# Kernel tuning notes

Hardware: AMD Instinct MI355X
Metric: run time of the kernel (lower is better)

Reference implementation:

```python
import jax, jax.numpy as jnp
import numpy as np

N = 4096  # num_neurons
THRESHOLD = 0.0  # torch forward default


def setup_inputs() -> dict:
    key = jax.random.key(0)
    k1, k2 = jax.random.split(key)
    W = jax.random.normal(k1, (N, N), dtype=jnp.float32)
    # Hopfield weights have zero self-connections (fill_diagonal_(0))
    W = W * (1.0 - jnp.eye(N, dtype=jnp.float32))
    x = jax.random.normal(k2, (N,), dtype=jnp.float32)
    return {"input_pattern": x, "weights": W, "max_iterations": 4}


def reference(input_pattern, weights, max_iterations):
    n = weights.shape[0]

    # One asynchronous neuron update: uses the CURRENT (partially updated) state.
    def neuron_step(state, i):
        activation = jnp.dot(weights[i], state)  # row-i dot current state
        state = state.at[i].set(jnp.sign(activation - THRESHOLD))
        return state, None

    # One full sweep over all neurons, in order 0..n-1 (asynchronous updates).
    def sweep(state, _):
        state, _ = jax.lax.scan(neuron_step, state, jnp.arange(n))
        return state, None

    # Fixed number of sweeps. A converged state is a fixed point of `sweep`,
    # so this matches the torch early-break loop's final output exactly.
    state, _ = jax.lax.scan(sweep, input_pattern, None, length=max_iterations)
    return state
```

## Files before the change

### kernel.cpp

```cpp
#include <hip/hip_runtime.h>

#define NN 4096
#define BB 128
#define GG 32
#define MAXT 8
#define MAXE (MAXT * GG)
#define MASK63 0x7FFFFFFFFFFFFFFFull
#define MASK62 0x3FFFFFFFFFFFFFFFull
#define TOPBIT 0x8000000000000000ull

__global__ __launch_bounds__(256)
void hop_init(const float* __restrict__ x, const float* __restrict__ W,
              unsigned long long* __restrict__ slots, float* __restrict__ partial_buf)
{
    const int tid = threadIdx.x, bid = blockIdx.x;
    const int lane = tid & 63, w = tid >> 6;
    const int lam = lane & 31, half = lane >> 5;

    if (bid == 0) {
        for (int i = tid; i < MAXE * 8; i += 256) slots[i] = 0ull;
    }

    const int tm = bid >> 3, tc = bid & 7;
    const int rbase = tm * BB, cbase = tc * 512;

    float4 xv[4];
#pragma unroll
    for (int u = 0; u < 4; ++u)
        xv[u] = *(const float4*)(x + cbase + 4 * lam + 128 * u);

#pragma unroll 2
    for (int it = 0; it < 16; ++it) {
        const int r = w * 32 + it * 2 + half;
        const float* wrow = W + (size_t)(rbase + r) * NN + cbase;
        float p = 0.f;
#pragma unroll
        for (int u = 0; u < 4; ++u) {
            float4 wv = *(const float4*)(wrow + 4 * lam + 128 * u);
            p = fmaf(wv.x, xv[u].x, p); p = fmaf(wv.y, xv[u].y, p);
            p = fmaf(wv.z, xv[u].z, p); p = fmaf(wv.w, xv[u].w, p);
        }
#pragma unroll
        for (int s = 16; s; s >>= 1) p += __shfl_xor(p, s);
        if (lam == 0) partial_buf[(size_t)bid * BB + r] = p;
    }
}

__global__ __launch_bounds__(256)
void hop_main(const float* __restrict__ x, const float* __restrict__ W,
              const int* __restrict__ maxit, float* __restrict__ out,
              unsigned long long* __restrict__ slots,
              const float* __restrict__ partial_buf)
{
    __shared__ float wdT[BB][BB + 1];
    __shared__ float a_lds[BB];
    __shared__ float prev_lds[NN];
    __shared__ float delta_lds[BB];
    __shared__ int   status_lds;
    __shared__ int   nzw[2][4];

    const int tid = threadIdx.x;
    const int m = blockIdx.x;
    const int lane = tid & 63, w = tid >> 6;
    const int lam = lane & 31, half = lane >> 5;
    const int bm = m * BB;

    int T = *maxit; if (T > MAXT) T = MAXT; if (T < 0) T = 0;
    const long long tstart = clock64();

    for (int l = tid; l < BB * BB; l += 256) {
        const int i = l >> 7, j = l & 127;
        wdT[j][i] = W[(size_t)(bm + i) * NN + bm + j];
    }
    for (int i = tid; i < NN; i += 256) prev_lds[i] = x[i];
    if (tid < BB) {
        float s = 0.f;
#pragma unroll
        for (int c = 0; c < 8; ++c) s += partial_buf[(size_t)(m * 8 + c) * BB + tid];
        a_lds[tid] = s;
    }
    float sold0 = 0.f, sold1 = 0.f;
    if (w == 0) { sold0 = x[bm + lane]; sold1 = x[bm + 64 + lane]; }
    __syncthreads();

    for (int e = 0; e < T * GG; ++e) {
        const int k = e & (GG - 1);
        if (k != m) {
            float4 wpre[16];
#pragma unroll
            for (int it = 0; it < 16; ++it) {
                const int r = w * 32 + it * 2 + half;
                wpre[it] = *(const float4*)(W + (size_t)(bm + r) * NN + k * BB + 4 * lam);
            }
            const unsigned long long* sl = slots + (size_t)e * 8;
            unsigned long long q0, q1, q2;
            int iters = 0;
            for (;;) {
                q0 = __hip_atomic_load(&sl[0], __ATOMIC_RELAXED, __HIP_MEMORY_SCOPE_AGENT);
                q1 = __hip_atomic_load(&sl[1], __ATOMIC_RELAXED, __HIP_MEMORY_SCOPE_AGENT);
                q2 = __hip_atomic_load(&sl[2], __ATOMIC_RELAXED, __HIP_MEMORY_SCOPE_AGENT);
                if ((q0 & q1 & q2) >> 63) break;
                __builtin_amdgcn_s_sleep(1);
                if (((++iters) & 255) == 0 && (clock64() - tstart) > 2000000000LL) break;
            }
            const unsigned long long m0 = (q0 & MASK63) | (q1 << 63);
            const unsigned long long m1 = ((q1 >> 1) & MASK62) | (q2 << 62);

            const int jc = 4 * lam;
            const float4 pv = *(const float4*)&prev_lds[k * BB + jc];
            float4 d4;
            {
                const float s0 = ((jc + 0 < 64 ? (m0 >> (jc + 0)) : (m1 >> (jc - 64))) & 1) ? 1.f : -1.f;
                const float s1 = ((jc + 1 < 64 ? (m0 >> (jc + 1)) : (m1 >> (jc - 63))) & 1) ? 1.f : -1.f;
                const float s2 = ((jc + 2 < 64 ? (m0 >> (jc + 2)) : (m1 >> (jc - 62))) & 1) ? 1.f : -1.f;
                const float s3 = ((jc + 3 < 64 ? (m0 >> (jc + 3)) : (m1 >> (jc - 61))) & 1) ? 1.f : -1.f;
                d4.x = s0 - pv.x; d4.y = s1 - pv.y; d4.z = s2 - pv.z; d4.w = s3 - pv.w;
            }
            const bool nz = (d4.x != 0.f) || (d4.y != 0.f) || (d4.z != 0.f) || (d4.w != 0.f);
            const unsigned long long bnz = __ballot(nz);
            if (lane == 0) nzw[e & 1][w] = (bnz != 0ull);
            __syncthreads();
            if (tid < BB) {
                const int b = tid < 64 ? (int)((m0 >> tid) & 1) : (int)((m1 >> (tid - 64)) & 1);
                prev_lds[k * BB + tid] = b ? 1.f : -1.f;
            }
            const int any = nzw[e & 1][0] | nzw[e & 1][1] | nzw[e & 1][2] | nzw[e & 1][3];
            if (any) {
#pragma unroll
                for (int it = 0; it < 16; ++it) {
                    const int r = w * 32 + it * 2 + half;
                    const float4 wv = wpre[it];
                    float p = fmaf(wv.x, d4.x, fmaf(wv.y, d4.y, fmaf(wv.z, d4.z, wv.w * d4.w)));
#pragma unroll
                    for (int s = 16; s; s >>= 1) p += __shfl_xor(p, s);
                    if (lam == 0) a_lds[r] += p;
                }
            }
        } else {
            __syncthreads();
            if (w == 0) {
                float c0 = a_lds[lane], c1 = a_lds[lane + 64];
                const float dp0 = 1.f - sold0, dm0 = -1.f - sold0;
                const float dp1 = 1.f - sold1, dm1 = -1.f - sold1;
                const float cand0 = c0 > 0.f ? dp0 : dm0;
                const float cand1 = c1 > 0.f ? dp1 : dm1;
                const unsigned long long bz = __ballot((cand0 != 0.f) || (cand1 != 0.f));
                float vdf0 = 0.f, vdf1 = 0.f;
                const int zero_all = (bz == 0ULL);
                if (!zero_all) {
                    float vsn0 = sold0, vsn1 = sold1;
                    float pw0[6], pw1[6];
#pragma unroll
                    for (int u = 0; u < 6; ++u) { pw0[u] = wdT[u][lane]; pw1[u] = wdT[u][lane + 64]; }
#pragma unroll
                    for (int j = 0; j < 64; ++j) {
                        const float dq = c0 > 0.f ? dp0 : dm0;
                        const float sq = c0 > 0.f ? 1.f : -1.f;
                        const float bc = __int_as_float(
                            __builtin_amdgcn_readlane(__float_as_int(dq), j));
                        const bool me = (lane == j);
                        vdf0 = me ? dq : vdf0;
                        vsn0 = me ? sq : vsn0;
                        const float w0 = pw0[j % 6], w1 = pw1[j % 6];
                        pw0[j % 6] = wdT[j + 6][lane];
                        pw1[j % 6] = wdT[j + 6][lane + 64];
                        c0 = fmaf(w0, bc, c0);
                        c1 = fmaf(w1, bc, c1);
                    }
                    const float cnd1 = c1 > 0.f ? dp1 : dm1;
                    const unsigned long long bz1 = __ballot(cnd1 != 0.f);
                    if (bz1 != 0ULL) {
#pragma unroll
                        for (int j = 64; j < 128; ++j) {
                            const float dq = c1 > 0.f ? dp1 : dm1;
                            const float sq = c1 > 0.f ? 1.f : -1.f;
                            const float bc = __int_as_float(
                                __builtin_amdgcn_readlane(__float_as_int(dq), j & 63));
                            const bool me = (lane == (j & 63));
                            vdf1 = me ? dq : vdf1;
                            vsn1 = me ? sq : vsn1;
                            const float w1 = pw1[j % 6];
                            if (j + 6 < BB) pw1[j % 6] = wdT[j + 6][lane + 64];
                            c1 = fmaf(w1, bc, c1);
                        }
                    }
                    sold0 = vsn0;
                    sold1 = vsn1;
                }
                {
                    const unsigned long long m0 = __ballot(sold0 > 0.f);
                    const unsigned long long m1 = __ballot(sold1 > 0.f);
                    unsigned long long* sl = slots + (size_t)e * 8;
                    if (lane == 0) {
                        __hip_atomic_store(&sl[0], TOPBIT | (m0 & MASK63),
                                           __ATOMIC_RELAXED, __HIP_MEMORY_SCOPE_AGENT);
                        __hip_atomic_store(&sl[1], TOPBIT | (m0 >> 63) | ((m1 & MASK62) << 1),
                                           __ATOMIC_RELAXED, __HIP_MEMORY_SCOPE_AGENT);
                        __hip_atomic_store(&sl[2], TOPBIT | (m1 >> 62),
                                           __ATOMIC_RELAXED, __HIP_MEMORY_SCOPE_AGENT);
                    }
                }
                if (lane == 0) status_lds = zero_all;
                if (!zero_all) {
                    delta_lds[lane] = vdf0;
                    delta_lds[lane + 64] = vdf1;
                }
            }
            __syncthreads();
            if (!status_lds) {
                float dv[4];
#pragma unroll
                for (int u = 0; u < 4; ++u) dv[u] = delta_lds[lam + 32 * u];
#pragma unroll 2
                for (int it = 0; it < 16; ++it) {
                    const int r = w * 32 + it * 2 + half;
                    float p = 0.f;
#pragma unroll
                    for (int u = 0; u < 4; ++u) p = fmaf(wdT[lam + 32 * u][r], dv[u], p);
#pragma unroll
                    for (int s = 16; s; s >>= 1) p += __shfl_xor(p, s);
                    if (lam == 0) a_lds[r] += p;
                }
            }
        }
    }

    if (w == 0) {
        out[bm + lane] = sold0;
        out[bm + 64 + lane] = sold1;
    }
}

extern "C" void kernel_launch(void* const* d_in, const int* in_sizes, int n_in,
                              void* d_out, int out_size, void* d_ws, size_t ws_size,
                              hipStream_t stream) {
    const float* x = (const float*)d_in[0];
    const float* W = (const float*)d_in[1];
    const int* maxit = (const int*)d_in[2];
    float* out = (float*)d_out;

    char* ws = (char*)d_ws;
    unsigned long long* slots = (unsigned long long*)ws;
    float* partial_buf = (float*)(ws + (size_t)MAXE * 8 * 8);
    if (ws_size < (size_t)(MAXE * 64 + 256 * BB * 4)) return;

    hipLaunchKernelGGL(hop_init, dim3(256), dim3(256), 0, stream,
                       x, W, slots, partial_buf);

    void* args[6];
    args[0] = (void*)&x; args[1] = (void*)&W; args[2] = (void*)&maxit;
    args[3] = (void*)&out; args[4] = (void*)&slots; args[5] = (void*)&partial_buf;
    (void)hipLaunchCooperativeKernel(hop_main, dim3(GG), dim3(256), args, 0u, stream);
}
```

Measured before the change: 1.103 ms.

## Poll slots from one wave with distance-scaled backoff and double-buffer prev state

Only wave 0 polls the global slot flags, and its sleep interval grows with the ring distance between producer and consumer block; the mask is then passed to the other waves through LDS after a barrier. The skip decision now compares the new mask with the previous sweep's mask kept in LDS, instead of a ballot over deltas and a second barrier. The previous-state array is double-buffered per sweep to avoid a read/write hazard. This aims to cut global polling traffic and barrier overhead on the serial chain, at the cost of more LDS and possible extra latency from longer sleeps.

Result: faster. 1.060 ms (-3.9%).

```diff
diff --git a/kernel.cpp b/kernel.cpp
--- a/kernel.cpp
+++ b/kernel.cpp
@@ -53,11 +53,12 @@
               const float* __restrict__ partial_buf)
 {
     __shared__ float wdT[BB][BB + 1];
+    __shared__ float pbuf[2][NN];
     __shared__ float a_lds[BB];
-    __shared__ float prev_lds[NN];
     __shared__ float delta_lds[BB];
+    __shared__ unsigned long long mbox[2][2];
+    __shared__ unsigned long long pm[2][GG][2];
     __shared__ int   status_lds;
-    __shared__ int   nzw[2][4];
 
     const int tid = threadIdx.x;
     const int m = blockIdx.x;
@@ -72,7 +73,7 @@
         const int i = l >> 7, j = l & 127;
         wdT[j][i] = W[(size_t)(bm + i) * NN + bm + j];
     }
-    for (int i = tid; i < NN; i += 256) prev_lds[i] = x[i];
+    for (int i = tid; i < NN; i += 256) pbuf[0][i] = x[i];
     if (tid < BB) {
         float s = 0.f;
 #pragma unroll
@@ -85,6 +86,7 @@
 
     for (int e = 0; e < T * GG; ++e) {
         const int k = e & (GG - 1);
+        const int s = e >> 5;
         if (k != m) {
             float4 wpre[16];
 #pragma unroll
@@ -92,22 +94,39 @@
                 const int r = w * 32 + it * 2 + half;
                 wpre[it] = *(const float4*)(W + (size_t)(bm + r) * NN + k * BB + 4 * lam);
             }
-            const unsigned long long* sl = slots + (size_t)e * 8;
-            unsigned long long q0, q1, q2;
-            int iters = 0;
-            for (;;) {
-                q0 = __hip_atomic_load(&sl[0], __ATOMIC_RELAXED, __HIP_MEMORY_SCOPE_AGENT);
-                q1 = __hip_atomic_load(&sl[1], __ATOMIC_RELAXED, __HIP_MEMORY_SCOPE_AGENT);
-                q2 = __hip_atomic_load(&sl[2], __ATOMIC_RELAXED, __HIP_MEMORY_SCOPE_AGENT);
-                if ((q0 & q1 & q2) >> 63) break;
-                __builtin_amdgcn_s_sleep(1);
-                if (((++iters) & 255) == 0 && (clock64() - tstart) > 2000000000LL) break;
-            }
-            const unsigned long long m0 = (q0 & MASK63) | (q1 << 63);
-            const unsigned long long m1 = ((q1 >> 1) & MASK62) | (q2 << 62);
+            if (w == 0) {
+                const unsigned long long* sl = slots + (size_t)e * 8;
+                const int dist = (m - k + GG) & (GG - 1);
+                unsigned long long q0, q1, q2;
+                long long iters = 0;
+                for (;;) {
+                    q0 = __hip_atomic_load(&sl[0], __ATOMIC_RELAXED, __HIP_MEMORY_SCOPE_AGENT);
+                    q1 = __hip_atomic_load(&sl[1], __ATOMIC_RELAXED, __HIP_MEMORY_SCOPE_AGENT);
+                    q2 = __hip_atomic_load(&sl[2], __ATOMIC_RELAXED, __HIP_MEMORY_SCOPE_AGENT);
+                    if ((q0 & q1 & q2) >> 63) break;
+                    if (dist == 1)      __builtin_amdgcn_s_sleep(1);
+                    else if (dist <= 4) __builtin_amdgcn_s_sleep(4);
+                    else                __builtin_amdgcn_s_sleep(32);
+                    if (((++iters) & 63) == 0 && (clock64() - tstart) > 500000000LL) break;
+                }
+                const unsigned long long mm0 = (q0 & MASK63) | (q1 << 63);
+                const unsigned long long mm1 = ((q1 >> 1) & MASK62) | (q2 << 62);
+                if (lane == 0) {
+                    mbox[e & 1][0] = mm0;
+                    mbox[e & 1][1] = mm1;
+                    pm[s & 1][k][0] = mm0;
+                    pm[s & 1][k][1] = mm1;
+                }
+            }
+            __syncthreads();
+            const unsigned long long m0 = mbox[e & 1][0];
+            const unsigned long long m1 = mbox[e & 1][1];
+            const bool any = (s == 0) ||
+                             (m0 != pm[(s - 1) & 1][k][0]) ||
+                             (m1 != pm[(s - 1) & 1][k][1]);
 
             const int jc = 4 * lam;
-            const float4 pv = *(const float4*)&prev_lds[k * BB + jc];
+            const float4 pv = *(const float4*)&pbuf[s & 1][k * BB + jc];
             float4 d4;
             {
                 const float s0 = ((jc + 0 < 64 ? (m0 >> (jc + 0)) : (m1 >> (jc - 64))) & 1) ? 1.f : -1.f;
@@ -116,15 +135,10 @@
                 const float s3 = ((jc + 3 < 64 ? (m0 >> (jc + 3)) : (m1 >> (jc - 61))) & 1) ? 1.f : -1.f;
                 d4.x = s0 - pv.x; d4.y = s1 - pv.y; d4.z = s2 - pv.z; d4.w = s3 - pv.w;
             }
-            const bool nz = (d4.x != 0.f) || (d4.y != 0.f) || (d4.z != 0.f) || (d4.w != 0.f);
-            const unsigned long long bnz = __ballot(nz);
-            if (lane == 0) nzw[e & 1][w] = (bnz != 0ull);
-            __syncthreads();
             if (tid < BB) {
                 const int b = tid < 64 ? (int)((m0 >> tid) & 1) : (int)((m1 >> (tid - 64)) & 1);
-                prev_lds[k * BB + tid] = b ? 1.f : -1.f;
-            }
-            const int any = nzw[e & 1][0] | nzw[e & 1][1] | nzw[e & 1][2] | nzw[e & 1][3];
+                pbuf[(s + 1) & 1][k * BB + tid] = b ? 1.f : -1.f;
+            }
             if (any) {
 #pragma unroll
                 for (int it = 0; it < 16; ++it) {
@@ -132,7 +146,7 @@
                     const float4 wv = wpre[it];
                     float p = fmaf(wv.x, d4.x, fmaf(wv.y, d4.y, fmaf(wv.z, d4.z, wv.w * d4.w)));
 #pragma unroll
-                    for (int s = 16; s; s >>= 1) p += __shfl_xor(p, s);
+                    for (int sh = 16; sh; sh >>= 1) p += __shfl_xor(p, sh);
                     if (lam == 0) a_lds[r] += p;
                 }
             }
@@ -188,15 +202,15 @@
                     sold1 = vsn1;
                 }
                 {
-                    const unsigned long long m0 = __ballot(sold0 > 0.f);
-                    const unsigned long long m1 = __ballot(sold1 > 0.f);
+                    const unsigned long long pm0 = __ballot(sold0 > 0.f);
+                    const unsigned long long pm1 = __ballot(sold1 > 0.f);
                     unsigned long long* sl = slots + (size_t)e * 8;
                     if (lane == 0) {
-                        __hip_atomic_store(&sl[0], TOPBIT | (m0 & MASK63),
+                        __hip_atomic_store(&sl[0], TOPBIT | (pm0 & MASK63),
                                            __ATOMIC_RELAXED, __HIP_MEMORY_SCOPE_AGENT);
-                        __hip_atomic_store(&sl[1], TOPBIT | (m0 >> 63) | ((m1 & MASK62) << 1),
+                        __hip_atomic_store(&sl[1], TOPBIT | (pm0 >> 63) | ((pm1 & MASK62) << 1),
                                            __ATOMIC_RELAXED, __HIP_MEMORY_SCOPE_AGENT);
-                        __hip_atomic_store(&sl[2], TOPBIT | (m1 >> 62),
+                        __hip_atomic_store(&sl[2], TOPBIT | (pm1 >> 62),
                                            __ATOMIC_RELAXED, __HIP_MEMORY_SCOPE_AGENT);
                     }
                 }
@@ -218,7 +232,7 @@
 #pragma unroll
                     for (int u = 0; u < 4; ++u) p = fmaf(wdT[lam + 32 * u][r], dv[u], p);
 #pragma unroll
-                    for (int s = 16; s; s >>= 1) p += __shfl_xor(p, s);
+                    for (int sh = 16; sh; sh >>= 1) p += __shfl_xor(p, sh);
                     if (lam == 0) a_lds[r] += p;
                 }
             }
```

## Use 8 large workgroups owning 4 sub-blocks each with pipelined delta application

Applied to the files above, without the earlier changes.

Switches from 32 workgroups of 256 threads, each owning one 128-row block, to 8 workgroups of 1024 threads, each owning 512 rows split into four 128-row sub-blocks. One wavefront polls the flag slots while the other 15 wavefronts apply the previous step's delta to the block's rows, so waiting and computation overlap. The next diagonal block is double-buffered into LDS during the serial update. Deltas are now formed from bitmasks of earlier states, and polling backs off according to how far away the producer is. The aim is fewer cross-workgroup handoffs and hidden polling latency, in exchange for reading W from global memory on every apply and having fewer CUs active.

After: 1.447 ms. +31.2%, slower.

```diff
diff --git a/kernel.cpp b/kernel.cpp
--- a/kernel.cpp
+++ b/kernel.cpp
@@ -1,10 +1,14 @@
 #include <hip/hip_runtime.h>
 
 #define NN 4096
-#define BB 128
-#define GG 32
+#define SB 128
+#define NSB 32
+#define NWG 8
+#define SPW 4
+#define ROWS 512
 #define MAXT 8
-#define MAXE (MAXT * GG)
+#define MAXE (MAXT * NSB)
+#define NTH 1024
 #define MASK63 0x7FFFFFFFFFFFFFFFull
 #define MASK62 0x3FFFFFFFFFFFFFFFull
 #define TOPBIT 0x8000000000000000ull
@@ -22,7 +26,7 @@
     }
 
     const int tm = bid >> 3, tc = bid & 7;
-    const int rbase = tm * BB, cbase = tc * 512;
+    const int rbase = tm * SB, cbase = tc * 512;
 
     float4 xv[4];
 #pragma unroll
@@ -42,104 +46,125 @@
         }
 #pragma unroll
         for (int s = 16; s; s >>= 1) p += __shfl_xor(p, s);
-        if (lam == 0) partial_buf[(size_t)bid * BB + r] = p;
-    }
-}
-
-__global__ __launch_bounds__(256)
+        if (lam == 0) partial_buf[(size_t)bid * SB + r] = p;
+    }
+}
+
+__device__ __forceinline__ void apply_rows(
+    const float* __restrict__ W, int rowbase, float* a_lds,
+    const float* dl_p, int cb, int r0, int r1, int wv, int lam, int half)
+{
+    const float4 d4 = *(const float4*)(dl_p + 4 * lam);
+    const int npairs = (r1 - r0) >> 1;
+    for (int i = wv - 1; i < npairs; i += 15) {
+        const int r = r0 + 2 * i + half;
+        const float* wr = W + (size_t)(rowbase + r) * NN + cb + 4 * lam;
+        const float4 wvv = *(const float4*)wr;
+        float p = fmaf(wvv.x, d4.x, fmaf(wvv.y, d4.y, fmaf(wvv.z, d4.z, wvv.w * d4.w)));
+#pragma unroll
+        for (int sh = 16; sh; sh >>= 1) p += __shfl_xor(p, sh);
+        if (lam == 0) a_lds[r] += p;
+    }
+}
+
+__global__ __launch_bounds__(NTH)
 void hop_main(const float* __restrict__ x, const float* __restrict__ W,
               const int* __restrict__ maxit, float* __restrict__ out,
               unsigned long long* __restrict__ slots,
               const float* __restrict__ partial_buf)
 {
-    __shared__ float wdT[BB][BB + 1];
-    __shared__ float a_lds[BB];
-    __shared__ float prev_lds[NN];
-    __shared__ float delta_lds[BB];
-    __shared__ int   status_lds;
-    __shared__ int   nzw[2][4];
+    __shared__ float wdT[2][SB][SB + 1];
+    __shared__ float x_lds[NN];
+    __shared__ float a_lds[ROWS];
+    __shared__ float sold_lds[ROWS];
+    __shared__ float dl[2][SB];
+    __shared__ unsigned long long pm[2][NSB][2];
+    __shared__ int pend_any[2];
+    __shared__ int pend_cb[2];
 
     const int tid = threadIdx.x;
     const int m = blockIdx.x;
-    const int lane = tid & 63, w = tid >> 6;
+    const int lane = tid & 63, wv = tid >> 6;
     const int lam = lane & 31, half = lane >> 5;
-    const int bm = m * BB;
+    const int rowbase = m * ROWS;
 
     int T = *maxit; if (T > MAXT) T = MAXT; if (T < 0) T = 0;
     const long long tstart = clock64();
 
-    for (int l = tid; l < BB * BB; l += 256) {
+    for (int i = tid; i < NN; i += NTH) x_lds[i] = x[i];
+    for (int l = tid; l < SB * SB; l += NTH) {
         const int i = l >> 7, j = l & 127;
-        wdT[j][i] = W[(size_t)(bm + i) * NN + bm + j];
-    }
-    for (int i = tid; i < NN; i += 256) prev_lds[i] = x[i];
-    if (tid < BB) {
+        wdT[0][j][i] = W[(size_t)(rowbase + i) * NN + rowbase + j];
+    }
+    if (tid < ROWS) {
         float s = 0.f;
 #pragma unroll
-        for (int c = 0; c < 8; ++c) s += partial_buf[(size_t)(m * 8 + c) * BB + tid];
+        for (int c = 0; c < 8; ++c)
+            s += partial_buf[(size_t)((m * SPW + (tid >> 7)) * 8 + c) * SB + (tid & 127)];
         a_lds[tid] = s;
-    }
-    float sold0 = 0.f, sold1 = 0.f;
-    if (w == 0) { sold0 = x[bm + lane]; sold1 = x[bm + 64 + lane]; }
+        sold_lds[tid] = x[rowbase + tid];
+    }
+    if (tid < 2) { pend_any[tid] = 0; pend_cb[tid] = 0; }
+    int cur = 0;
     __syncthreads();
 
-    for (int e = 0; e < T * GG; ++e) {
-        const int k = e & (GG - 1);
-        if (k != m) {
-            float4 wpre[16];
-#pragma unroll
-            for (int it = 0; it < 16; ++it) {
-                const int r = w * 32 + it * 2 + half;
-                wpre[it] = *(const float4*)(W + (size_t)(bm + r) * NN + k * BB + 4 * lam);
+    for (int t = 0; t < T * NSB; ++t) {
+        const int b = t & (NSB - 1);
+        const int s = t >> 5;
+        const int pp = t & 1, qq = pp ^ 1;
+        if ((b >> 2) != m) {
+            if (wv == 0) {
+                const unsigned long long* sl = slots + (size_t)t * 8;
+                const int d = (b < SPW * m) ? (SPW * m - b) : (NSB - b + SPW * m);
+                unsigned long long q0, q1, q2;
+                long long iters = 0;
+                for (;;) {
+                    q0 = __hip_atomic_load(&sl[0], __ATOMIC_RELAXED, __HIP_MEMORY_SCOPE_AGENT);
+                    q1 = __hip_atomic_load(&sl[1], __ATOMIC_RELAXED, __HIP_MEMORY_SCOPE_AGENT);
+                    q2 = __hip_atomic_load(&sl[2], __ATOMIC_RELAXED, __HIP_MEMORY_SCOPE_AGENT);
+                    if ((q0 & q1 & q2) >> 63) break;
+                    if (d == 1)      __builtin_amdgcn_s_sleep(1);
+                    else if (d <= 4) __builtin_amdgcn_s_sleep(4);
+                    else             __builtin_amdgcn_s_sleep(32);
+                    if (((++iters) & 63) == 0 && (clock64() - tstart) > 500000000LL) break;
+                }
+                const unsigned long long mm0 = (q0 & MASK63) | (q1 << 63);
+                const unsigned long long mm1 = ((q1 >> 1) & MASK62) | (q2 << 62);
+                const unsigned long long p0 = pm[(s - 1) & 1][b][0];
+                const unsigned long long p1 = pm[(s - 1) & 1][b][1];
+                const int any = (s == 0) || (mm0 != p0) || (mm1 != p1);
+                {
+                    const int j0 = lane;
+                    const float cur0 = ((mm0 >> j0) & 1) ? 1.f : -1.f;
+                    const float prev0 = (s == 0) ? x_lds[b * SB + j0]
+                                                 : (((p0 >> j0) & 1) ? 1.f : -1.f);
+                    dl[pp][j0] = cur0 - prev0;
+                    const float cur1 = ((mm1 >> j0) & 1) ? 1.f : -1.f;
+                    const float prev1 = (s == 0) ? x_lds[b * SB + 64 + j0]
+                                                 : (((p1 >> j0) & 1) ? 1.f : -1.f);
+                    dl[pp][64 + j0] = cur1 - prev1;
+                }
+                if (lane == 0) {
+                    pm[s & 1][b][0] = mm0;
+                    pm[s & 1][b][1] = mm1;
+                    pend_any[pp] = any;
+                    pend_cb[pp] = b * SB;
+                }
+            } else {
+                if (pend_any[qq])
+                    apply_rows(W, rowbase, a_lds, dl[qq], pend_cb[qq], 0, ROWS, wv, lam, half);
             }
-            const unsigned long long* sl = slots + (size_t)e * 8;
-            unsigned long long q0, q1, q2;
-            int iters = 0;
-            for (;;) {
-                q0 = __hip_atomic_load(&sl[0], __ATOMIC_RELAXED, __HIP_MEMORY_SCOPE_AGENT);
-                q1 = __hip_atomic_load(&sl[1], __ATOMIC_RELAXED, __HIP_MEMORY_SCOPE_AGENT);
-                q2 = __hip_atomic_load(&sl[2], __ATOMIC_RELAXED, __HIP_MEMORY_SCOPE_AGENT);
-                if ((q0 & q1 & q2) >> 63) break;
-                __builtin_amdgcn_s_sleep(1);
-                if (((++iters) & 255) == 0 && (clock64() - tstart) > 2000000000LL) break;
-            }
-            const unsigned long long m0 = (q0 & MASK63) | (q1 << 63);
-            const unsigned long long m1 = ((q1 >> 1) & MASK62) | (q2 << 62);
-
-            const int jc = 4 * lam;
-            const float4 pv = *(const float4*)&prev_lds[k * BB + jc];
-            float4 d4;
-            {
-                const float s0 = ((jc + 0 < 64 ? (m0 >> (jc + 0)) : (m1 >> (jc - 64))) & 1) ? 1.f : -1.f;
-                const float s1 = ((jc + 1 < 64 ? (m0 >> (jc + 1)) : (m1 >> (jc - 63))) & 1) ? 1.f : -1.f;
-                const float s2 = ((jc + 2 < 64 ? (m0 >> (jc + 2)) : (m1 >> (jc - 62))) & 1) ? 1.f : -1.f;
-                const float s3 = ((jc + 3 < 64 ? (m0 >> (jc + 3)) : (m1 >> (jc - 61))) & 1) ? 1.f : -1.f;
-                d4.x = s0 - pv.x; d4.y = s1 - pv.y; d4.z = s2 - pv.z; d4.w = s3 - pv.w;
-            }
-            const bool nz = (d4.x != 0.f) || (d4.y != 0.f) || (d4.z != 0.f) || (d4.w != 0.f);
-            const unsigned long long bnz = __ballot(nz);
-            if (lane == 0) nzw[e & 1][w] = (bnz != 0ull);
             __syncthreads();
-            if (tid < BB) {
-                const int b = tid < 64 ? (int)((m0 >> tid) & 1) : (int)((m1 >> (tid - 64)) & 1);
-                prev_lds[k * BB + tid] = b ? 1.f : -1.f;
-            }
-            const int any = nzw[e & 1][0] | nzw[e & 1][1] | nzw[e & 1][2] | nzw[e & 1][3];
-            if (any) {
-#pragma unroll
-                for (int it = 0; it < 16; ++it) {
-                    const int r = w * 32 + it * 2 + half;
-                    const float4 wv = wpre[it];
-                    float p = fmaf(wv.x, d4.x, fmaf(wv.y, d4.y, fmaf(wv.z, d4.z, wv.w * d4.w)));
-#pragma unroll
-                    for (int s = 16; s; s >>= 1) p += __shfl_xor(p, s);
-                    if (lam == 0) a_lds[r] += p;
-                }
-            }
         } else {
+            const int lb = b & (SPW - 1);
+            if (wv > 0 && pend_any[qq])
+                apply_rows(W, rowbase, a_lds, dl[qq], pend_cb[qq],
+                           lb * SB, lb * SB + SB, wv, lam, half);
             __syncthreads();
-            if (w == 0) {
-                float c0 = a_lds[lane], c1 = a_lds[lane + 64];
+            if (wv == 0) {
+                float (*wd)[SB + 1] = wdT[cur];
+                float c0 = a_lds[lb * SB + lane], c1 = a_lds[lb * SB + 64 + lane];
+                float sold0 = sold_lds[lb * SB + lane], sold1 = sold_lds[lb * SB + 64 + lane];
                 const float dp0 = 1.f - sold0, dm0 = -1.f - sold0;
                 const float dp1 = 1.f - sold1, dm1 = -1.f - sold1;
                 const float cand0 = c0 > 0.f ? dp0 : dm0;
@@ -151,7 +176,7 @@
                     float vsn0 = sold0, vsn1 = sold1;
                     float pw0[6], pw1[6];
 #pragma unroll
-                    for (int u = 0; u < 6; ++u) { pw0[u] = wdT[u][lane]; pw1[u] = wdT[u][lane + 64]; }
+                    for (int u = 0; u < 6; ++u) { pw0[u] = wd[u][lane]; pw1[u] = wd[u][lane + 64]; }
 #pragma unroll
                     for (int j = 0; j < 64; ++j) {
                         const float dq = c0 > 0.f ? dp0 : dm0;
@@ -162,8 +187,8 @@
                         vdf0 = me ? dq : vdf0;
                         vsn0 = me ? sq : vsn0;
                         const float w0 = pw0[j % 6], w1 = pw1[j % 6];
-                        pw0[j % 6] = wdT[j + 6][lane];
-                        pw1[j % 6] = wdT[j + 6][lane + 64];
+                        pw0[j % 6] = wd[j + 6][lane];
+                        pw1[j % 6] = wd[j + 6][lane + 64];
                         c0 = fmaf(w0, bc, c0);
                         c1 = fmaf(w1, bc, c1);
                     }
@@ -180,55 +205,50 @@
                             vdf1 = me ? dq : vdf1;
                             vsn1 = me ? sq : vsn1;
                             const float w1 = pw1[j % 6];
-                            if (j + 6 < BB) pw1[j % 6] = wdT[j + 6][lane + 64];
+                            if (j + 6 < SB) pw1[j % 6] = wd[j + 6][lane + 64];
                             c1 = fmaf(w1, bc, c1);
                         }
                     }
-                    sold0 = vsn0;
-                    sold1 = vsn1;
+                    sold0 = vsn0; sold1 = vsn1;
+                    sold_lds[lb * SB + lane] = sold0;
+                    sold_lds[lb * SB + 64 + lane] = sold1;
                 }
                 {
-                    const unsigned long long m0 = __ballot(sold0 > 0.f);
-                    const unsigned long long m1 = __ballot(sold1 > 0.f);
-                    unsigned long long* sl = slots + (size_t)e * 8;
+                    const unsigned long long b0 = __ballot(sold0 > 0.f);
+                    const unsigned long long b1 = __ballot(sold1 > 0.f);
+                    unsigned long long* sl = slots + (size_t)t * 8;
                     if (lane == 0) {
-                        __hip_atomic_store(&sl[0], TOPBIT | (m0 & MASK63),
+                        __hip_atomic_store(&sl[0], TOPBIT | (b0 & MASK63),
                                            __ATOMIC_RELAXED, __HIP_MEMORY_SCOPE_AGENT);
-                        __hip_atomic_store(&sl[1], TOPBIT | (m0 >> 63) | ((m1 & MASK62) << 1),
+                        __hip_atomic_store(&sl[1], TOPBIT | (b0 >> 63) | ((b1 & MASK62) << 1),
                                            __ATOMIC_RELAXED, __HIP_MEMORY_SCOPE_AGENT);
-                        __hip_atomic_store(&sl[2], TOPBIT | (m1 >> 62),
+                        __hip_atomic_store(&sl[2], TOPBIT | (b1 >> 62),
                                            __ATOMIC_RELAXED, __HIP_MEMORY_SCOPE_AGENT);
                     }
                 }
-                if (lane == 0) status_lds = zero_all;
-                if (!zero_all) {
-                    delta_lds[lane] = vdf0;
-                    delta_lds[lane + 64] = vdf1;
+                dl[pp][lane] = vdf0;
+                dl[pp][lane + 64] = vdf1;
+                if (lane == 0) { pend_any[pp] = !zero_all; pend_cb[pp] = b * SB; }
+            } else {
+                if (pend_any[qq]) {
+                    apply_rows(W, rowbase, a_lds, dl[qq], pend_cb[qq],
+                               0, lb * SB, wv, lam, half);
+                    apply_rows(W, rowbase, a_lds, dl[qq], pend_cb[qq],
+                               lb * SB + SB, ROWS, wv, lam, half);
+                }
+                const int nlb = (lb + 1) & (SPW - 1);
+                const int nb = rowbase + nlb * SB;
+                for (int l = tid - 64; l < SB * SB; l += (NTH - 64)) {
+                    const int i = l >> 7, j = l & 127;
+                    wdT[cur ^ 1][j][i] = W[(size_t)(nb + i) * NN + nb + j];
                 }
             }
             __syncthreads();
-            if (!status_lds) {
-                float dv[4];
-#pragma unroll
-                for (int u = 0; u < 4; ++u) dv[u] = delta_lds[lam + 32 * u];
-#pragma unroll 2
-                for (int it = 0; it < 16; ++it) {
-                    const int r = w * 32 + it * 2 + half;
-                    float p = 0.f;
-#pragma unroll
-                    for (int u = 0; u < 4; ++u) p = fmaf(wdT[lam + 32 * u][r], dv[u], p);
-#pragma unroll
-                    for (int s = 16; s; s >>= 1) p += __shfl_xor(p, s);
-                    if (lam == 0) a_lds[r] += p;
-                }
-            }
+            cur ^= 1;
         }
     }
 
-    if (w == 0) {
-        out[bm + lane] = sold0;
-        out[bm + 64 + lane] = sold1;
-    }
+    if (tid < ROWS) out[rowbase + tid] = sold_lds[tid];
 }
 
 extern "C" void kernel_launch(void* const* d_in, const int* in_sizes, int n_in,
@@ -241,8 +261,8 @@
 
     char* ws = (char*)d_ws;
     unsigned long long* slots = (unsigned long long*)ws;
-    float* partial_buf = (float*)(ws + (size_t)MAXE * 8 * 8);
-    if (ws_size < (size_t)(MAXE * 64 + 256 * BB * 4)) return;
+    float* partial_buf = (float*)(ws + (size_t)MAXE * 64);
+    if (ws_size < (size_t)(MAXE * 64 + 256 * SB * 4)) return;
 
     hipLaunchKernelGGL(hop_init, dim3(256), dim3(256), 0, stream,
                        x, W, slots, partial_buf);
@@ -250,5 +270,5 @@
     void* args[6];
     args[0] = (void*)&x; args[1] = (void*)&W; args[2] = (void*)&maxit;
     args[3] = (void*)&out; args[4] = (void*)&slots; args[5] = (void*)&partial_buf;
-    (void)hipLaunchCooperativeKernel(hop_main, dim3(GG), dim3(256), args, 0u, stream);
-}
+    (void)hipLaunchCooperativeKernel(hop_main, dim3(NWG), dim3(NTH), args, 0u, stream);
+}
```
